# Kernel tuning notes

Measured on AMD Instinct MI355X. Metric: run time of the kernel, lower is better.

The kernel has to match this reference:

```python
import jax, jax.numpy as jnp
import numpy as np

# camera / raster constants
N = 10000            # gaussians
W = 256
H = 256
FX = 200.0
FY = 200.0
TILE = 16
NTX = W // TILE
NTY = H // TILE
NT = NTX * NTY       # 256 tiles
P = TILE * TILE      # 256 pixels per tile
K = 256              # max gaussians kept per tile
NEAR = 0.3
MAGIC = 1.2          # frustum expansion factor from project_culling
LP = 0.3 / (FX * FX) # low-pass filter added to 2D covariance diagonal


def quat_to_rot(q):
    w, x, y, z = q[:, 0], q[:, 1], q[:, 2], q[:, 3]
    r0 = jnp.stack([1 - 2 * (y * y + z * z), 2 * (x * y - w * z), 2 * (x * z + w * y)], -1)
    r1 = jnp.stack([2 * (x * y + w * z), 1 - 2 * (x * x + z * z), 2 * (y * z - w * x)], -1)
    r2 = jnp.stack([2 * (x * z - w * y), 2 * (y * z + w * x), 1 - 2 * (x * x + y * y)], -1)
    return jnp.stack([r0, r1, r2], axis=1)  # [N,3,3]


def splat_forward(pos, rgb, opacity, quaternion, scale, w2c_r, w2c_t):
    # ---- project + frustum cull (global_culling) ----
    q = quaternion / jnp.linalg.norm(quaternion, axis=-1, keepdims=True)
    R = quat_to_rot(q)
    sigma = jnp.exp(scale)                               # normalize_scale
    cov3d = jnp.einsum('nij,nj,nkj->nik', R, sigma * sigma, R)
    p_cam = pos @ w2c_r.T + w2c_t                        # [N,3]
    x, y, z = p_cam[:, 0], p_cam[:, 1], p_cam[:, 2]
    zc = jnp.maximum(z, 1e-6)
    half_w = W * MAGIC / 2 / FX
    half_h = H * MAGIC / 2 / FY
    mean2d = jnp.stack([x / zc, y / zc], -1)             # camera-plane coords
    in_frustum = (z > NEAR) & (jnp.abs(mean2d[:, 0]) < half_w) & (jnp.abs(mean2d[:, 1]) < half_h)
    iz = 1.0 / zc
    zero = jnp.zeros_like(iz)
    J = jnp.stack([jnp.stack([iz, zero, -x * iz * iz], -1),
                   jnp.stack([zero, iz, -y * iz * iz], -1)], axis=1)  # [N,2,3]
    cov_cam = jnp.einsum('ij,njk,lk->nil', w2c_r, cov3d, w2c_r)
    cov2d = jnp.einsum('nij,njk,nlk->nil', J, cov_cam, J)            # [N,2,2]
    a = cov2d[:, 0, 0] + LP
    c = cov2d[:, 1, 1] + LP
    b = cov2d[:, 0, 1]

    # ---- per-tile culling + fixed-K binning (calc_tile_list / gather_gaussians) ----
    cx = (jnp.arange(NTX) * TILE + TILE / 2 - W / 2) / FX
    cy = (jnp.arange(NTY) * TILE + TILE / 2 - H / 2) / FY
    centers = jnp.stack(jnp.meshgrid(cx, cy, indexing='xy'), -1).reshape(NT, 2)  # [NT,2] (ty-major)
    tile_half_diag = 0.5 * jnp.sqrt((TILE / FX) ** 2 + (TILE / FY) ** 2)
    mid = 0.5 * (a + c)
    sigma_max = jnp.sqrt(jnp.maximum(mid + jnp.sqrt(jnp.maximum((0.5 * (a - c)) ** 2 + b * b, 0.0)), 1e-12))
    dist = jnp.linalg.norm(centers[:, None, :] - mean2d[None, :, :], axis=-1)   # [NT,N]
    valid = in_frustum[None, :] & (dist <= (3.0 * sigma_max + tile_half_diag)[None, :])
    score = jnp.where(valid, -dist, -1e10)
    vals, idx = jax.lax.top_k(score, K)                                          # [NT,K]
    valid_k = vals > -1e9

    mean_g = mean2d[idx]                     # [NT,K,2]
    z_g = z[idx]
    a_g, b_g, c_g = a[idx], b[idx], c[idx]
    opa_g = jax.nn.sigmoid(opacity)[idx]
    rgb_g = jax.nn.sigmoid(rgb)[idx]         # [NT,K,3]

    # ---- depth sort within each tile ----
    order = jnp.argsort(jnp.where(valid_k, z_g, jnp.inf), axis=-1)
    def srt(arr):
        o = order.reshape(order.shape + (1,) * (arr.ndim - 2))
        return jnp.take_along_axis(arr, o, axis=1)
    mean_s, a_s, b_s, c_s = srt(mean_g), srt(a_g), srt(b_g), srt(c_g)
    opa_s, rgb_s = srt(opa_g), srt(rgb_g)
    valid_s = srt(valid_k).astype(pos.dtype)

    # ---- per-pixel front-to-back alpha compositing (draw) ----
    px = ((jnp.arange(W) + 0.5 - W / 2) / FX).reshape(NTX, TILE)
    py = ((jnp.arange(H) + 0.5 - H / 2) / FY).reshape(NTY, TILE)
    U = jnp.broadcast_to(px[None, :, None, :], (NTY, NTX, TILE, TILE)).reshape(NT, P)
    V = jnp.broadcast_to(py[:, None, :, None], (NTY, NTX, TILE, TILE)).reshape(NT, P)
    dx = U[:, :, None] - mean_s[:, None, :, 0]          # [NT,P,K]
    dy = V[:, :, None] - mean_s[:, None, :, 1]
    det = jnp.maximum(a_s * c_s - b_s * b_s, 1e-12)[:, None, :]
    maha = (c_s[:, None, :] * dx * dx - 2.0 * b_s[:, None, :] * dx * dy + a_s[:, None, :] * dy * dy) / det
    alpha = jnp.clip(opa_s[:, None, :] * jnp.exp(-0.5 * maha), 0.0, 0.99) * valid_s[:, None, :]
    trans = jnp.cumprod(1.0 - alpha, axis=-1)
    texc = jnp.concatenate([jnp.ones_like(trans[..., :1]), trans[..., :-1]], axis=-1)
    color = jnp.einsum('tpk,tkc->tpc', alpha * texc, rgb_s)  # [NT,P,3]
    img = color.reshape(NTY, NTX, TILE, TILE, 3).transpose(0, 2, 1, 3, 4).reshape(H, W, 3)
    return jnp.clip(img, 0.0, 1.0)


def setup_inputs() -> dict:
    key = jax.random.key(0)
    ks = jax.random.split(key, 6)
    zpos = jax.random.uniform(ks[0], (N,), minval=2.0, maxval=6.0)
    uv = jax.random.uniform(ks[1], (N, 2), minval=-0.6, maxval=0.6)
    pos = jnp.concatenate([uv * zpos[:, None], zpos[:, None]], axis=-1)
    rgb = jax.random.normal(ks[2], (N, 3))              # pre-sigmoid logits
    opacity = jax.random.normal(ks[3], (N,)) + 1.5      # sigmoid -> ~0.8 like init_opacity
    quaternion = jax.random.normal(ks[4], (N, 4))
    scale = 0.2 * jax.random.normal(ks[5], (N, 3)) - 4.5  # exp -> ~0.01 world sigma
    w2c_r = jnp.eye(3, dtype=jnp.float32)
    w2c_t = jnp.zeros((3,), dtype=jnp.float32)
    return {"pos": pos, "rgb": rgb, "opacity": opacity, "quaternion": quaternion,
            "scale": scale, "w2c_r": w2c_r, "w2c_t": w2c_t}


def reference(pos, rgb, opacity, quaternion, scale, w2c_r, w2c_t):
    return splat_forward(pos, rgb, opacity, quaternion, scale, w2c_r, w2c_t)
```

## Files before the change

### kernel.cpp

```cpp
#include <hip/hip_runtime.h>
#include <math.h>

namespace {
constexpr int W = 256, H = 256, TILE = 16, NTX = 16, NT = 256, K = 256;
constexpr float FX = 200.0f, FY = 200.0f, NEARP = 0.3f, MAGIC = 1.2f;
constexpr float LP = 0.3f / (FX * FX);
constexpr float HALF_W = W * MAGIC / 2.0f / FX;
constexpr float HALF_H = H * MAGIC / 2.0f / FY;
constexpr float THDIAG = 0.05656854249492381f;
constexpr int CAP = 2048;
constexpr int N_PAD = 10240;
constexpr int BT = 1024;
constexpr size_t A_OFF = 0;
constexpr size_t B_OFF = A_OFF + (size_t)N_PAD * 16;
constexpr size_t C_OFF = B_OFF + (size_t)N_PAD * 16;
}


__global__ __launch_bounds__(256)
void preprocess_k(const float* __restrict__ pos, const float* __restrict__ rgb,
                  const float* __restrict__ opac, const float* __restrict__ quat,
                  const float* __restrict__ scl, const float* __restrict__ w2cr,
                  const float* __restrict__ w2ct,
                  float4* __restrict__ pa, float4* __restrict__ pb,
                  float4* __restrict__ pc, int n) {
  int g = blockIdx.x * 256 + (int)threadIdx.x;
  if (g >= n) return;
  float p0 = pos[3*g+0], p1 = pos[3*g+1], p2 = pos[3*g+2];
  float qw = quat[4*g+0], qx = quat[4*g+1], qy = quat[4*g+2], qz = quat[4*g+3];
  float inv = 1.0f / sqrtf(qw*qw + qx*qx + qy*qy + qz*qz);
  qw *= inv; qx *= inv; qy *= inv; qz *= inv;
  float r00 = 1.f-2.f*(qy*qy+qz*qz), r01 = 2.f*(qx*qy-qw*qz), r02 = 2.f*(qx*qz+qw*qy);
  float r10 = 2.f*(qx*qy+qw*qz), r11 = 1.f-2.f*(qx*qx+qz*qz), r12 = 2.f*(qy*qz-qw*qx);
  float r20 = 2.f*(qx*qz-qw*qy), r21 = 2.f*(qy*qz+qw*qx), r22 = 1.f-2.f*(qx*qx+qy*qy);
  float e0 = expf(scl[3*g+0]); float s0 = e0*e0;
  float e1 = expf(scl[3*g+1]); float s1 = e1*e1;
  float e2 = expf(scl[3*g+2]); float s2 = e2*e2;
  float C00 = r00*r00*s0 + r01*r01*s1 + r02*r02*s2;
  float C01 = r00*r10*s0 + r01*r11*s1 + r02*r12*s2;
  float C02 = r00*r20*s0 + r01*r21*s1 + r02*r22*s2;
  float C11 = r10*r10*s0 + r11*r11*s1 + r12*r12*s2;
  float C12 = r10*r20*s0 + r11*r21*s1 + r12*r22*s2;
  float C22 = r20*r20*s0 + r21*r21*s1 + r22*r22*s2;
  float w00=w2cr[0],w01=w2cr[1],w02=w2cr[2];
  float w10=w2cr[3],w11=w2cr[4],w12=w2cr[5];
  float w20=w2cr[6],w21=w2cr[7],w22=w2cr[8];
  float x = w00*p0 + w01*p1 + w02*p2 + w2ct[0];
  float y = w10*p0 + w11*p1 + w12*p2 + w2ct[1];
  float z = w20*p0 + w21*p1 + w22*p2 + w2ct[2];
  float m00 = w00*C00 + w01*C01 + w02*C02;
  float m01 = w00*C01 + w01*C11 + w02*C12;
  float m02 = w00*C02 + w01*C12 + w02*C22;
  float m10 = w10*C00 + w11*C01 + w12*C02;
  float m11 = w10*C01 + w11*C11 + w12*C12;
  float m12 = w10*C02 + w11*C12 + w12*C22;
  float m20 = w20*C00 + w21*C01 + w22*C02;
  float m21 = w20*C01 + w21*C11 + w22*C12;
  float m22 = w20*C02 + w21*C12 + w22*C22;
  float v00 = m00*w00 + m01*w01 + m02*w02;
  float v01 = m00*w10 + m01*w11 + m02*w12;
  float v02 = m00*w20 + m01*w21 + m02*w22;
  float v10 = m10*w00 + m11*w01 + m12*w02;
  float v11 = m10*w10 + m11*w11 + m12*w12;
  float v12 = m10*w20 + m11*w21 + m12*w22;
  float v20 = m20*w00 + m21*w01 + m22*w02;
  float v21 = m20*w10 + m21*w11 + m22*w12;
  float v22 = m20*w20 + m21*w21 + m22*w22;
  float zc = fmaxf(z, 1e-6f);
  float iz = 1.0f / zc;
  float mx = x * iz, my = y * iz;
  float iz2 = iz * iz;
  float jx = -x * iz2, jy = -y * iz2;
  float a00 = iz*v00 + jx*v20, a01 = iz*v01 + jx*v21, a02 = iz*v02 + jx*v22;
  float a10 = iz*v10 + jy*v20, a11 = iz*v11 + jy*v21, a12 = iz*v12 + jy*v22;
  float A  = a00*iz + a02*jx + LP;
  float Bv = a01*iz + a02*jy;
  float Cv = a11*iz + a12*jy + LP;
  float mid = 0.5f*(A + Cv);
  float hh  = 0.5f*(A - Cv);
  float disc = fmaxf(hh*hh + Bv*Bv, 0.0f);
  float smax = sqrtf(fmaxf(mid + sqrtf(disc), 1e-12f));
  bool infr = (z > NEARP) && (fabsf(mx) < HALF_W) && (fabsf(my) < HALF_H);
  float radius = infr ? (3.0f * smax + THDIAG) : -1.0f;
  float det = fmaxf(A * Cv - Bv * Bv, 1e-12f);
  pa[g] = make_float4(mx, my, radius, z);
  pb[g] = make_float4(A, Bv, Cv, 1.0f / det);
  pc[g] = make_float4(1.0f / (1.0f + __expf(-opac[g])),
                      1.0f / (1.0f + __expf(-rgb[3*g+0])),
                      1.0f / (1.0f + __expf(-rgb[3*g+1])),
                      1.0f / (1.0f + __expf(-rgb[3*g+2])));
}


template <int S>
__device__ inline void hsortN(unsigned long long* key, int M) {
  const int tid = (int)threadIdx.x;
  __syncthreads();
  unsigned long long e[S];
  #pragma unroll
  for (int s = 0; s < S; ++s) {
    int i = tid + (s << 10);
    e[s] = (i < M) ? key[i] : ~0ull;
  }
  for (int k = 2; k <= M; k <<= 1) {
    for (int j = k >> 1; j >= 64; j >>= 1) {
      __syncthreads();
      #pragma unroll
      for (int s = 0; s < S; ++s) {
        int i = tid + (s << 10);
        if (i < M) key[i] = e[s];
      }
      __syncthreads();
      #pragma unroll
      for (int s = 0; s < S; ++s) {
        int i = tid + (s << 10);
        if (i < M) {
          unsigned long long p = key[i ^ j];
          bool takeMin = (((i & j) == 0) == ((i & k) == 0));
          e[s] = ((p < e[s]) == takeMin) ? p : e[s];
        }
      }
    }
    int j0 = ((k >> 1) < 32) ? (k >> 1) : 32;
    for (int j = j0; j >= 1; j >>= 1) {
      #pragma unroll
      for (int s = 0; s < S; ++s) {
        int i = tid + (s << 10);
        unsigned long long p = __shfl_xor(e[s], j, 64);
        bool takeMin = (((i & j) == 0) == ((i & k) == 0));
        e[s] = ((p < e[s]) == takeMin) ? p : e[s];
      }
    }
  }
  __syncthreads();
  #pragma unroll
  for (int s = 0; s < S; ++s) {
    int i = tid + (s << 10);
    if (i < M) key[i] = e[s];
  }
  __syncthreads();
}


__global__ __launch_bounds__(BT)
void render_k(const float4* __restrict__ pa, const float4* __restrict__ pb,
              const float4* __restrict__ pc, float* __restrict__ out, int n) {
  __shared__ unsigned long long s_dkey[CAP];
  __shared__ unsigned long long s_zkey[CAP];
  __shared__ int s_rank[K];
  __shared__ float4 s_p0[K];
  __shared__ float4 s_p1[K];
  __shared__ float2 s_p2[K];
  __shared__ float4 s_part[BT];
  __shared__ int s_cnt;

  const int t  = (int)blockIdx.x;
  const int tx = t % NTX;
  const int ty = t / NTX;
  const int tid = (int)threadIdx.x;
  const int lane = tid & 63;
  const float cxc = (tx * TILE + TILE * 0.5f - W * 0.5f) / FX;
  const float cyc = (ty * TILE + TILE * 0.5f - H * 0.5f) / FY;

  if (tid == 0) s_cnt = 0;
  if (tid < K) s_rank[tid] = 0;
  __syncthreads();

  for (int g = tid; g < n; g += BT) {
    float4 v = pa[g];
    float ddx = cxc - v.x, ddy = cyc - v.y;
    float dist = sqrtf(ddx * ddx + ddy * ddy);
    bool hit = (v.z >= 0.0f) && (dist <= v.z);
    unsigned long long m = __ballot(hit);
    if (m) {
      int leader = __ffsll((long long)m) - 1;
      int base = 0;
      if (lane == leader) base = atomicAdd(&s_cnt, __popcll(m));
      base = __shfl(base, leader, 64);
      if (hit) {
        int slot = base + __popcll(m & ((1ull << lane) - 1ull));
        if (slot < CAP) {
          s_dkey[slot] = ((unsigned long long)__float_as_uint(dist) << 32) |
                         (unsigned int)g;
          s_zkey[slot] = ((unsigned long long)__float_as_uint(v.w) << 32) |
                         (unsigned int)g;
        }
      }
    }
  }
  __syncthreads();
  int cnt = min(s_cnt, CAP);
  int cnt2 = cnt;

  if (cnt > K) {
    int M = 512; while (M < cnt) M <<= 1;
    for (int i = cnt + tid; i < M; i += BT) s_dkey[i] = ~0ull;
    if (M <= 1024) hsortN<1>(s_dkey, M);
    else           hsortN<2>(s_dkey, 2048);
    if (tid < K) {
      int g = (int)(s_dkey[tid] & 0xffffffffu);
      s_zkey[tid] = ((unsigned long long)__float_as_uint(pa[g].w) << 32) |
                    (unsigned int)g;
    }
    __syncthreads();
    cnt2 = K;
  }

  {
    const int e = tid & 255;
    const int q = tid >> 8;
    if (e < cnt2) {
      unsigned long long mykey = s_zkey[e];
      int jlo = q * 64;
      int jhi = min(cnt2, jlo + 64);
      int partial = 0;
      for (int j = jlo; j < jhi; ++j)
        partial += (s_zkey[j] < mykey) ? 1 : 0;
      if (partial) atomicAdd(&s_rank[e], partial);
    }
  }
  __syncthreads();

  if (tid < cnt2) {
    int g = (int)(s_zkey[tid] & 0xffffffffu);
    int r = s_rank[tid];
    float4 A = pa[g], B = pb[g], C = pc[g];
    s_p0[r] = make_float4(A.x, A.y, B.x, B.y);
    s_p1[r] = make_float4(B.z, B.w, C.x, C.y);
    s_p2[r] = make_float2(C.z, C.w);
  }
  __syncthreads();

  const int p    = tid & 255;
  const int q    = tid >> 8;
  const int prow = p / TILE, pcol = p % TILE;
  const float u = ((float)(tx * TILE + pcol) + 0.5f - W * 0.5f) / FX;
  const float v = ((float)(ty * TILE + prow) + 0.5f - H * 0.5f) / FY;
  const int chunk = (cnt2 + 3) >> 2;
  const int k0 = q * chunk;
  const int k1 = min(cnt2, k0 + chunk);
  float T = 1.0f, accr = 0.0f, accg = 0.0f, accb = 0.0f;
  for (int k2 = k0; k2 < k1; ++k2) {
    float4 p0 = s_p0[k2];
    float4 p1 = s_p1[k2];
    float2 p2 = s_p2[k2];
    float dx = u - p0.x;
    float dy = v - p0.y;
    float maha = (p1.x*dx*dx - 2.0f*p0.w*dx*dy + p0.z*dy*dy) * p1.y;
    float alpha = fminf(p1.z * __expf(-0.5f * maha), 0.99f);
    float w = alpha * T;
    accr += w * p1.w;
    accg += w * p2.x;
    accb += w * p2.y;
    T *= (1.0f - alpha);
  }
  s_part[tid] = make_float4(accr, accg, accb, T);
  __syncthreads();

  if (q == 0) {
    float4 P0 = s_part[p];
    float4 P1 = s_part[p + 256];
    float4 P2 = s_part[p + 512];
    float4 P3 = s_part[p + 768];
    float r = P0.x + P0.w * (P1.x + P1.w * (P2.x + P2.w * P3.x));
    float g = P0.y + P0.w * (P1.y + P1.w * (P2.y + P2.w * P3.y));
    float b = P0.z + P0.w * (P1.z + P1.w * (P2.z + P2.w * P3.z));
    const int row = ty * TILE + prow;
    const int col = tx * TILE + pcol;
    const int o = (row * W + col) * 3;
    out[o+0] = fminf(fmaxf(r, 0.0f), 1.0f);
    out[o+1] = fminf(fmaxf(g, 0.0f), 1.0f);
    out[o+2] = fminf(fmaxf(b, 0.0f), 1.0f);
  }
}

extern "C" void kernel_launch(void* const* d_in, const int* in_sizes, int n_in,
                              void* d_out, int out_size, void* d_ws, size_t ws_size,
                              hipStream_t stream) {
  const float* pos  = (const float*)d_in[0];
  const float* rgb  = (const float*)d_in[1];
  const float* opac = (const float*)d_in[2];
  const float* quat = (const float*)d_in[3];
  const float* scl  = (const float*)d_in[4];
  const float* w2cr = (const float*)d_in[5];
  const float* w2ct = (const float*)d_in[6];
  float* out = (float*)d_out;
  const int n = in_sizes[0] / 3;

  char* ws = (char*)d_ws;
  float4* pa = (float4*)(ws + A_OFF);
  float4* pb = (float4*)(ws + B_OFF);
  float4* pc = (float4*)(ws + C_OFF);
  preprocess_k<<<(n + 255) / 256, 256, 0, stream>>>(
      pos, rgb, opac, quat, scl, w2cr, w2ct, pa, pb, pc, n);
  render_k<<<NT, BT, 0, stream>>>(pa, pb, pc, out, n);
}
```

Measured before the change: 26.44 us.

## Bin gaussians into per-tile segment lists during preprocess instead of full scans

Preprocessing now computes each gaussian's tile bounding range, tests tile-center distance, and appends dist/z keys into per-(tile, source block) segments with shared-memory counters. The render kernel prefix-sums the segment lengths and gathers only the listed candidates. Each tile block therefore no longer scans all N gaussians. In exchange it needs a large workspace and scattered global writes, and falls back to the old scan path when the workspace is too small. Segment overflow is not guarded (SEG=256 per block per tile).

```diff
diff --git a/kernel.cpp b/kernel.cpp
--- a/kernel.cpp
+++ b/kernel.cpp
@@ -11,21 +11,24 @@
 constexpr int CAP = 2048;
 constexpr int N_PAD = 10240;
 constexpr int BT = 1024;
-constexpr size_t A_OFF = 0;
-constexpr size_t B_OFF = A_OFF + (size_t)N_PAD * 16;
-constexpr size_t C_OFF = B_OFF + (size_t)N_PAD * 16;
-}
-
-
-__global__ __launch_bounds__(256)
-void preprocess_k(const float* __restrict__ pos, const float* __restrict__ rgb,
-                  const float* __restrict__ opac, const float* __restrict__ quat,
-                  const float* __restrict__ scl, const float* __restrict__ w2cr,
-                  const float* __restrict__ w2ct,
-                  float4* __restrict__ pa, float4* __restrict__ pb,
-                  float4* __restrict__ pc, int n) {
-  int g = blockIdx.x * 256 + (int)threadIdx.x;
-  if (g >= n) return;
+constexpr int NB_MAX = 64;
+constexpr int SEG = 256;
+constexpr size_t A_OFF  = 0;
+constexpr size_t B_OFF  = A_OFF + (size_t)N_PAD * 16;
+constexpr size_t C_OFF  = B_OFF + (size_t)N_PAD * 16;
+constexpr size_t SL_OFF = C_OFF + (size_t)N_PAD * 16;
+constexpr size_t LD_OFF = SL_OFF + (size_t)NT * NB_MAX * 4;
+constexpr size_t LZ_OFF = LD_OFF + (size_t)NT * NB_MAX * SEG * 8;
+constexpr size_t WS_FULL = LZ_OFF + (size_t)NT * NB_MAX * SEG * 8;
+}
+
+struct Pre { float mx, my, z, a, b, c, radius; };
+
+__device__ inline Pre preprocess(int g, const float* __restrict__ pos,
+                                 const float* __restrict__ quat,
+                                 const float* __restrict__ scl,
+                                 const float* __restrict__ w2cr,
+                                 const float* __restrict__ w2ct) {
   float p0 = pos[3*g+0], p1 = pos[3*g+1], p2 = pos[3*g+2];
   float qw = quat[4*g+0], qx = quat[4*g+1], qy = quat[4*g+2], qz = quat[4*g+3];
   float inv = 1.0f / sqrtf(qw*qw + qx*qx + qy*qy + qz*qz);
@@ -81,14 +84,69 @@
   float disc = fmaxf(hh*hh + Bv*Bv, 0.0f);
   float smax = sqrtf(fmaxf(mid + sqrtf(disc), 1e-12f));
   bool infr = (z > NEARP) && (fabsf(mx) < HALF_W) && (fabsf(my) < HALF_H);
-  float radius = infr ? (3.0f * smax + THDIAG) : -1.0f;
-  float det = fmaxf(A * Cv - Bv * Bv, 1e-12f);
-  pa[g] = make_float4(mx, my, radius, z);
-  pb[g] = make_float4(A, Bv, Cv, 1.0f / det);
-  pc[g] = make_float4(1.0f / (1.0f + __expf(-opac[g])),
-                      1.0f / (1.0f + __expf(-rgb[3*g+0])),
-                      1.0f / (1.0f + __expf(-rgb[3*g+1])),
-                      1.0f / (1.0f + __expf(-rgb[3*g+2])));
+  Pre r;
+  r.mx = mx; r.my = my; r.z = z; r.a = A; r.b = Bv; r.c = Cv;
+  r.radius = infr ? (3.0f * smax + THDIAG) : -1.0f;
+  return r;
+}
+
+
+template <bool BIN>
+__global__ __launch_bounds__(256)
+void pre_bin(const float* __restrict__ pos, const float* __restrict__ rgb,
+             const float* __restrict__ opac, const float* __restrict__ quat,
+             const float* __restrict__ scl, const float* __restrict__ w2cr,
+             const float* __restrict__ w2ct,
+             float4* __restrict__ pa, float4* __restrict__ pb,
+             float4* __restrict__ pc, int* __restrict__ seglen,
+             unsigned long long* __restrict__ listd,
+             unsigned long long* __restrict__ listz, int n) {
+  __shared__ int s_tc[NT];
+  const int tid = (int)threadIdx.x;
+  const int blk = (int)blockIdx.x;
+  if (BIN) {
+    if (tid < NT) s_tc[tid] = 0;
+    __syncthreads();
+  }
+  const int g = blk * 256 + tid;
+  if (g < n) {
+    Pre p = preprocess(g, pos, quat, scl, w2cr, w2ct);
+    float det = fmaxf(p.a * p.c - p.b * p.b, 1e-12f);
+    pa[g] = make_float4(p.mx, p.my, p.radius, p.z);
+    pb[g] = make_float4(p.a, p.b, p.c, 1.0f / det);
+    pc[g] = make_float4(1.0f / (1.0f + __expf(-opac[g])),
+                        1.0f / (1.0f + __expf(-rgb[3*g+0])),
+                        1.0f / (1.0f + __expf(-rgb[3*g+1])),
+                        1.0f / (1.0f + __expf(-rgb[3*g+2])));
+    if (BIN && p.radius >= 0.0f) {
+      float r = p.radius;
+      int txlo = max(0,     (int)floorf(((p.mx - r) * FX + 120.0f) * 0.0625f));
+      int txhi = min(NTX-1, (int)ceilf (((p.mx + r) * FX + 120.0f) * 0.0625f));
+      int tylo = max(0,     (int)floorf(((p.my - r) * FY + 120.0f) * 0.0625f));
+      int tyhi = min(NTX-1, (int)ceilf (((p.my + r) * FY + 120.0f) * 0.0625f));
+      unsigned long long gbits = (unsigned int)g;
+      for (int ty = tylo; ty <= tyhi; ++ty) {
+        float cy = (ty * TILE + TILE * 0.5f - H * 0.5f) / FY;
+        float ddy = cy - p.my;
+        for (int tx = txlo; tx <= txhi; ++tx) {
+          float cx = (tx * TILE + TILE * 0.5f - W * 0.5f) / FX;
+          float ddx = cx - p.mx;
+          float dist = sqrtf(ddx * ddx + ddy * ddy);
+          if (dist <= r) {
+            int t = ty * NTX + tx;
+            int slot = atomicAdd(&s_tc[t], 1);
+            size_t idx = ((size_t)t * NB_MAX + blk) * SEG + slot;
+            listd[idx] = ((unsigned long long)__float_as_uint(dist) << 32) | gbits;
+            listz[idx] = ((unsigned long long)__float_as_uint(p.z)  << 32) | gbits;
+          }
+        }
+      }
+    }
+  }
+  if (BIN) {
+    __syncthreads();
+    if (tid < NT) seglen[(size_t)tid * NB_MAX + blk] = s_tc[tid];
+  }
 }
 
 
@@ -142,70 +200,13 @@
 }
 
 
-__global__ __launch_bounds__(BT)
-void render_k(const float4* __restrict__ pa, const float4* __restrict__ pb,
-              const float4* __restrict__ pc, float* __restrict__ out, int n) {
-  __shared__ unsigned long long s_dkey[CAP];
-  __shared__ unsigned long long s_zkey[CAP];
-  __shared__ int s_rank[K];
-  __shared__ float4 s_p0[K];
-  __shared__ float4 s_p1[K];
-  __shared__ float2 s_p2[K];
-  __shared__ float4 s_part[BT];
-  __shared__ int s_cnt;
-
-  const int t  = (int)blockIdx.x;
-  const int tx = t % NTX;
-  const int ty = t / NTX;
+__device__ inline void sort_blend_store(
+    const float4* __restrict__ pa, const float4* __restrict__ pb,
+    const float4* __restrict__ pc, float* __restrict__ out,
+    unsigned long long* s_zkey, int* s_rank,
+    float4* s_p0, float4* s_p1, float2* s_p2, float4* s_part,
+    int cnt2, int tx, int ty) {
   const int tid = (int)threadIdx.x;
-  const int lane = tid & 63;
-  const float cxc = (tx * TILE + TILE * 0.5f - W * 0.5f) / FX;
-  const float cyc = (ty * TILE + TILE * 0.5f - H * 0.5f) / FY;
-
-  if (tid == 0) s_cnt = 0;
-  if (tid < K) s_rank[tid] = 0;
-  __syncthreads();
-
-  for (int g = tid; g < n; g += BT) {
-    float4 v = pa[g];
-    float ddx = cxc - v.x, ddy = cyc - v.y;
-    float dist = sqrtf(ddx * ddx + ddy * ddy);
-    bool hit = (v.z >= 0.0f) && (dist <= v.z);
-    unsigned long long m = __ballot(hit);
-    if (m) {
-      int leader = __ffsll((long long)m) - 1;
-      int base = 0;
-      if (lane == leader) base = atomicAdd(&s_cnt, __popcll(m));
-      base = __shfl(base, leader, 64);
-      if (hit) {
-        int slot = base + __popcll(m & ((1ull << lane) - 1ull));
-        if (slot < CAP) {
-          s_dkey[slot] = ((unsigned long long)__float_as_uint(dist) << 32) |
-                         (unsigned int)g;
-          s_zkey[slot] = ((unsigned long long)__float_as_uint(v.w) << 32) |
-                         (unsigned int)g;
-        }
-      }
-    }
-  }
-  __syncthreads();
-  int cnt = min(s_cnt, CAP);
-  int cnt2 = cnt;
-
-  if (cnt > K) {
-    int M = 512; while (M < cnt) M <<= 1;
-    for (int i = cnt + tid; i < M; i += BT) s_dkey[i] = ~0ull;
-    if (M <= 1024) hsortN<1>(s_dkey, M);
-    else           hsortN<2>(s_dkey, 2048);
-    if (tid < K) {
-      int g = (int)(s_dkey[tid] & 0xffffffffu);
-      s_zkey[tid] = ((unsigned long long)__float_as_uint(pa[g].w) << 32) |
-                    (unsigned int)g;
-    }
-    __syncthreads();
-    cnt2 = K;
-  }
-
   {
     const int e = tid & 255;
     const int q = tid >> 8;
@@ -220,7 +221,6 @@
     }
   }
   __syncthreads();
-
   if (tid < cnt2) {
     int g = (int)(s_zkey[tid] & 0xffffffffu);
     int r = s_rank[tid];
@@ -230,7 +230,6 @@
     s_p2[r] = make_float2(C.z, C.w);
   }
   __syncthreads();
-
   const int p    = tid & 255;
   const int q    = tid >> 8;
   const int prow = p / TILE, pcol = p % TILE;
@@ -256,7 +255,6 @@
   }
   s_part[tid] = make_float4(accr, accg, accb, T);
   __syncthreads();
-
   if (q == 0) {
     float4 P0 = s_part[p];
     float4 P1 = s_part[p + 256];
@@ -274,6 +272,141 @@
   }
 }
 
+
+__global__ __launch_bounds__(BT)
+void render_list(const float4* __restrict__ pa, const float4* __restrict__ pb,
+                 const float4* __restrict__ pc, const int* __restrict__ seglen,
+                 const unsigned long long* __restrict__ listd,
+                 const unsigned long long* __restrict__ listz,
+                 float* __restrict__ out, int nb) {
+  __shared__ unsigned long long s_dkey[CAP];
+  __shared__ unsigned long long s_zkey[CAP];
+  __shared__ int s_off[NB_MAX + 1];
+  __shared__ int s_rank[K];
+  __shared__ float4 s_p0[K];
+  __shared__ float4 s_p1[K];
+  __shared__ float2 s_p2[K];
+  __shared__ float4 s_part[BT];
+
+  const int t  = (int)blockIdx.x;
+  const int tx = t % NTX;
+  const int ty = t / NTX;
+  const int tid = (int)threadIdx.x;
+
+  if (tid < K) s_rank[tid] = 0;
+  if (tid < 64) {
+    int v = (tid < nb) ? seglen[(size_t)t * NB_MAX + tid] : 0;
+    #pragma unroll
+    for (int d = 1; d < 64; d <<= 1) {
+      int u2 = __shfl_up(v, d, 64);
+      if (tid >= d) v += u2;
+    }
+    if (tid == 0) s_off[0] = 0;
+    if (tid < nb) s_off[tid + 1] = v;
+  }
+  __syncthreads();
+  int cnt = min(s_off[nb], CAP);
+
+  for (int i = tid; i < cnt; i += BT) {
+    int lo = 0, hi = nb;
+    while (hi - lo > 1) {
+      int mid = (lo + hi) >> 1;
+      if (s_off[mid] <= i) lo = mid; else hi = mid;
+    }
+    size_t src = ((size_t)t * NB_MAX + lo) * SEG + (size_t)(i - s_off[lo]);
+    s_dkey[i] = listd[src];
+    s_zkey[i] = listz[src];
+  }
+  __syncthreads();
+  int cnt2 = cnt;
+
+  if (cnt > K) {
+    int M = 512; while (M < cnt) M <<= 1;
+    for (int i = cnt + tid; i < M; i += BT) s_dkey[i] = ~0ull;
+    if (M <= 1024) hsortN<1>(s_dkey, M);
+    else           hsortN<2>(s_dkey, 2048);
+    if (tid < K) {
+      int g = (int)(s_dkey[tid] & 0xffffffffu);
+      s_zkey[tid] = ((unsigned long long)__float_as_uint(pa[g].w) << 32) |
+                    (unsigned int)g;
+    }
+    __syncthreads();
+    cnt2 = K;
+  }
+
+  sort_blend_store(pa, pb, pc, out, s_zkey, s_rank, s_p0, s_p1, s_p2, s_part,
+                   cnt2, tx, ty);
+}
+
+
+__global__ __launch_bounds__(BT)
+void render_scan(const float4* __restrict__ pa, const float4* __restrict__ pb,
+                 const float4* __restrict__ pc, float* __restrict__ out, int n) {
+  __shared__ unsigned long long s_dkey[CAP];
+  __shared__ unsigned long long s_zkey[CAP];
+  __shared__ int s_rank[K];
+  __shared__ float4 s_p0[K];
+  __shared__ float4 s_p1[K];
+  __shared__ float2 s_p2[K];
+  __shared__ float4 s_part[BT];
+  __shared__ int s_cnt;
+
+  const int t  = (int)blockIdx.x;
+  const int tx = t % NTX;
+  const int ty = t / NTX;
+  const int tid = (int)threadIdx.x;
+  const int lane = tid & 63;
+  const float cxc = (tx * TILE + TILE * 0.5f - W * 0.5f) / FX;
+  const float cyc = (ty * TILE + TILE * 0.5f - H * 0.5f) / FY;
+
+  if (tid == 0) s_cnt = 0;
+  if (tid < K) s_rank[tid] = 0;
+  __syncthreads();
+
+  for (int g = tid; g < n; g += BT) {
+    float4 v = pa[g];
+    float ddx = cxc - v.x, ddy = cyc - v.y;
+    float dist = sqrtf(ddx * ddx + ddy * ddy);
+    bool hit = (v.z >= 0.0f) && (dist <= v.z);
+    unsigned long long m = __ballot(hit);
+    if (m) {
+      int leader = __ffsll((long long)m) - 1;
+      int base = 0;
+      if (lane == leader) base = atomicAdd(&s_cnt, __popcll(m));
+      base = __shfl(base, leader, 64);
+      if (hit) {
+        int slot = base + __popcll(m & ((1ull << lane) - 1ull));
+        if (slot < CAP) {
+          s_dkey[slot] = ((unsigned long long)__float_as_uint(dist) << 32) |
+                         (unsigned int)g;
+          s_zkey[slot] = ((unsigned long long)__float_as_uint(v.w) << 32) |
+                         (unsigned int)g;
+        }
+      }
+    }
+  }
+  __syncthreads();
+  int cnt = min(s_cnt, CAP);
+  int cnt2 = cnt;
+
+  if (cnt > K) {
+    int M = 512; while (M < cnt) M <<= 1;
+    for (int i = cnt + tid; i < M; i += BT) s_dkey[i] = ~0ull;
+    if (M <= 1024) hsortN<1>(s_dkey, M);
+    else           hsortN<2>(s_dkey, 2048);
+    if (tid < K) {
+      int g = (int)(s_dkey[tid] & 0xffffffffu);
+      s_zkey[tid] = ((unsigned long long)__float_as_uint(pa[g].w) << 32) |
+                    (unsigned int)g;
+    }
+    __syncthreads();
+    cnt2 = K;
+  }
+
+  sort_blend_store(pa, pb, pc, out, s_zkey, s_rank, s_p0, s_p1, s_p2, s_part,
+                   cnt2, tx, ty);
+}
+
 extern "C" void kernel_launch(void* const* d_in, const int* in_sizes, int n_in,
                               void* d_out, int out_size, void* d_ws, size_t ws_size,
                               hipStream_t stream) {
@@ -286,12 +419,23 @@
   const float* w2ct = (const float*)d_in[6];
   float* out = (float*)d_out;
   const int n = in_sizes[0] / 3;
+  const int nb = (n + 255) / 256;
 
   char* ws = (char*)d_ws;
   float4* pa = (float4*)(ws + A_OFF);
   float4* pb = (float4*)(ws + B_OFF);
   float4* pc = (float4*)(ws + C_OFF);
-  preprocess_k<<<(n + 255) / 256, 256, 0, stream>>>(
-      pos, rgb, opac, quat, scl, w2cr, w2ct, pa, pb, pc, n);
-  render_k<<<NT, BT, 0, stream>>>(pa, pb, pc, out, n);
-}
+  int* seglen = (int*)(ws + SL_OFF);
+  unsigned long long* listd = (unsigned long long*)(ws + LD_OFF);
+  unsigned long long* listz = (unsigned long long*)(ws + LZ_OFF);
+
+  if (ws_size >= WS_FULL && nb <= NB_MAX) {
+    pre_bin<true><<<nb, 256, 0, stream>>>(
+        pos, rgb, opac, quat, scl, w2cr, w2ct, pa, pb, pc, seglen, listd, listz, n);
+    render_list<<<NT, BT, 0, stream>>>(pa, pb, pc, seglen, listd, listz, out, nb);
+  } else {
+    pre_bin<false><<<nb, 256, 0, stream>>>(
+        pos, rgb, opac, quat, scl, w2cr, w2ct, pa, pb, pc, seglen, listd, listz, n);
+    render_scan<<<NT, BT, 0, stream>>>(pa, pb, pc, out, n);
+  }
+}
```

Result: faster. 24.99 us (-5.5%).
